# Kernel tuning notes

Measured on AMD Instinct MI355X. Metric: run time of the kernel, lower is better.

Reference implementation:

```python
import jax, jax.numpy as jnp
import numpy as np

TEMPERATURE = 0.2
HYPER_GAMMA = 0.5
EPS = 1e-12  # torch F.normalize / cosine_similarity eps guard (1e-12 / 1e-8)

def setup_inputs() -> dict:
    key = jax.random.key(0)
    k1, k2 = jax.random.split(key)
    B, D = 4096, 1024
    return {
        "emb_i": jax.random.normal(k1, (B, D), dtype=jnp.float32),
        "emb_j": jax.random.normal(k2, (B, D), dtype=jnp.float32),
    }

def _l2_normalize(x, eps=EPS):
    n = jnp.sqrt(jnp.sum(x * x, axis=1, keepdims=True))
    return x / jnp.maximum(n, eps)

def reference(emb_i, emb_j):
    B = emb_i.shape[0]
    z_i = _l2_normalize(emb_i)
    z_j = _l2_normalize(emb_j)
    # cosine similarity of unit vectors == dot product; sim[a, b] = <z_j[a], z_i[b]>
    sim = jnp.einsum('ad,bd->ab', z_j, z_i)  # [B, B]
    sim_positive = jnp.diagonal(sim)
    positives_exp = jnp.exp(-sim_positive + TEMPERATURE)
    neg_mask = 1.0 - jnp.eye(B, dtype=sim.dtype)
    negatives_exp = neg_mask * jnp.exp(sim - TEMPERATURE)
    positives_sum = jnp.sum(jnp.log1p(positives_exp)) / B
    negatives_sum = jnp.sum(jnp.log1p(negatives_exp)) / (B * (B - 1))
    return HYPER_GAMMA * positives_sum + (1.0 - HYPER_GAMMA) * negatives_sum
```

## Files before the change

kernel.cpp:

```cpp
#include <hip/hip_runtime.h>
#include <math.h>

#define B_ROWS 4096
#define D_DIM  1024
static constexpr float TEMP = 0.2f;
static constexpr float FP8_SCALE = 16.0f;
static constexpr float INV_S2 = 1.0f / 256.0f;

typedef __attribute__((ext_vector_type(4))) float f32x4;

__device__ inline unsigned char f2fp8(float f) {
    unsigned int u = __float_as_uint(f);
    unsigned int s = (u >> 24) & 0x80u;
    float af = fabsf(f);
    unsigned char b;
    if (af >= 0x1.0p-6f) {
        unsigned int au = u & 0x7fffffffu;
        unsigned int lsb = (au >> 20) & 1u;
        au += 0x7ffffu + lsb;
        int e = (int)(au >> 23) - 127 + 7;
        unsigned int m = (au >> 20) & 7u;
        if (e > 15 || (e == 15 && m > 6)) b = 0x7e;
        else b = (unsigned char)((e << 3) | m);
    } else {
        int q = (int)rintf(af * 512.0f);
        b = (unsigned char)(q >= 8 ? 0x08 : q);
    }
    return (unsigned char)(b | s);
}

__device__ inline unsigned int f2fp8x4(float4 v) {
    return (unsigned int)f2fp8(v.x)
         | ((unsigned int)f2fp8(v.y) << 8)
         | ((unsigned int)f2fp8(v.z) << 16)
         | ((unsigned int)f2fp8(v.w) << 24);
}

__device__ inline void gload_lds16(const unsigned char* g, unsigned char* l) {
    __builtin_amdgcn_global_load_lds(
        (const __attribute__((address_space(1))) unsigned int*)g,
        (__attribute__((address_space(3))) unsigned int*)l,
        16, 0, 0);
}


__global__ __launch_bounds__(256) void norm_cast_kernel(
        const float* __restrict__ emb_i, const float* __restrict__ emb_j,
        unsigned char* __restrict__ Zi8, unsigned char* __restrict__ Zj8,
        float* __restrict__ w) {
    const int tid = threadIdx.x;
    if (blockIdx.x == 0 && tid == 0) {
        w[0] = 0.0f; w[1] = 0.0f;
        ((unsigned int*)w)[2] = 0u;
    }
    const int wave = tid >> 6, lane = tid & 63;
    const int row = blockIdx.x * 4 + wave;
    const float* src; unsigned char* dst; int r;
    if (row < B_ROWS) { src = emb_i; dst = Zi8; r = row; }
    else              { src = emb_j; dst = Zj8; r = row - B_ROWS; }

    const float4* p = (const float4*)(src + (size_t)r * D_DIM);
    float4 v0 = p[lane], v1 = p[64 + lane], v2 = p[128 + lane], v3 = p[192 + lane];
    float s = v0.x*v0.x + v0.y*v0.y + v0.z*v0.z + v0.w*v0.w
            + v1.x*v1.x + v1.y*v1.y + v1.z*v1.z + v1.w*v1.w
            + v2.x*v2.x + v2.y*v2.y + v2.z*v2.z + v2.w*v2.w
            + v3.x*v3.x + v3.y*v3.y + v3.z*v3.z + v3.w*v3.w;
    #pragma unroll
    for (int m = 1; m < 64; m <<= 1) s += __shfl_xor(s, m, 64);
    const float inv = FP8_SCALE / fmaxf(sqrtf(s), 1e-12f);

    float4 a0 = {v0.x*inv, v0.y*inv, v0.z*inv, v0.w*inv};
    float4 a1 = {v1.x*inv, v1.y*inv, v1.z*inv, v1.w*inv};
    float4 a2 = {v2.x*inv, v2.y*inv, v2.z*inv, v2.w*inv};
    float4 a3 = {v3.x*inv, v3.y*inv, v3.z*inv, v3.w*inv};
    unsigned int* q = (unsigned int*)(dst + (size_t)r * D_DIM);
    q[lane]       = f2fp8x4(a0);
    q[64 + lane]  = f2fp8x4(a1);
    q[128 + lane] = f2fp8x4(a2);
    q[192 + lane] = f2fp8x4(a3);
}

__global__ __launch_bounds__(256, 2) void simloss_mfma_fp8_kernel(
        const unsigned char* __restrict__ Zi8,
        const unsigned char* __restrict__ Zj8,
        float* __restrict__ w, float* __restrict__ out) {
    __shared__ __align__(16) unsigned char lA[128 * 64];
    __shared__ __align__(16) unsigned char lB[256 * 64];
    __shared__ float rn[4], rp[4];

    const int tid  = threadIdx.x;
    const int lane = tid & 63;
    const int wave = tid >> 6;
    const int wy = wave >> 1, wx = wave & 1;
    const int rowBase = blockIdx.y * 128;
    const int colBase = blockIdx.x * 256;

    const int lrow = lane >> 2;
    const int lp   = lane & 3;
    const int lc   = (lp - (lrow >> 2)) & 3;
    const unsigned char* gA0 = Zj8 + (size_t)(rowBase + (2*wave+0)*16 + lrow) * D_DIM + lc*16;
    const unsigned char* gA1 = Zj8 + (size_t)(rowBase + (2*wave+1)*16 + lrow) * D_DIM + lc*16;
    const unsigned char* gB0 = Zi8 + (size_t)(colBase + (4*wave+0)*16 + lrow) * D_DIM + lc*16;
    const unsigned char* gB1 = Zi8 + (size_t)(colBase + (4*wave+1)*16 + lrow) * D_DIM + lc*16;
    const unsigned char* gB2 = Zi8 + (size_t)(colBase + (4*wave+2)*16 + lrow) * D_DIM + lc*16;
    const unsigned char* gB3 = Zi8 + (size_t)(colBase + (4*wave+3)*16 + lrow) * D_DIM + lc*16;
    unsigned char* sA0 = lA + (2*wave+0) * 1024;
    unsigned char* sA1 = lA + (2*wave+1) * 1024;
    unsigned char* sB0 = lB + (4*wave+0) * 1024;
    unsigned char* sB1 = lB + (4*wave+1) * 1024;
    unsigned char* sB2 = lB + (4*wave+2) * 1024;
    unsigned char* sB3 = lB + (4*wave+3) * 1024;

    const int fr = lane & 15;
    const int q4 = lane >> 4;
    const int qh = q4 >> 1, qb = q4 & 1;
    const int P0 = (qh + 0 + (fr >> 2)) & 3;
    const int P1 = (qh + 2 + (fr >> 2)) & 3;
    const unsigned char* fA0 = lA + (wy * 64 + fr) * 64 + P0 * 16 + qb * 8;
    const unsigned char* fA1 = lA + (wy * 64 + fr) * 64 + P1 * 16 + qb * 8;
    const unsigned char* fB0 = lB + (wx * 128 + fr) * 64 + P0 * 16 + qb * 8;
    const unsigned char* fB1 = lB + (wx * 128 + fr) * 64 + P1 * 16 + qb * 8;

    f32x4 acc[4][8];
    #pragma unroll
    for (int i = 0; i < 4; ++i)
        #pragma unroll
        for (int j = 0; j < 8; ++j)
            acc[i][j] = (f32x4){0.f, 0.f, 0.f, 0.f};

    for (int k0 = 0; k0 < D_DIM; k0 += 64) {
        __syncthreads();
        gload_lds16(gA0, sA0); gload_lds16(gA1, sA1);
        gload_lds16(gB0, sB0); gload_lds16(gB1, sB1);
        gload_lds16(gB2, sB2); gload_lds16(gB3, sB3);
        gA0 += 64; gA1 += 64; gB0 += 64; gB1 += 64; gB2 += 64; gB3 += 64;
        __syncthreads();

        {
            long a[4], b[8];
            #pragma unroll
            for (int i = 0; i < 4; ++i) a[i] = *(const long*)(fA0 + i * 1024);
            #pragma unroll
            for (int j = 0; j < 8; ++j) b[j] = *(const long*)(fB0 + j * 1024);
            #pragma unroll
            for (int i = 0; i < 4; ++i)
                #pragma unroll
                for (int j = 0; j < 8; ++j)
                    acc[i][j] = __builtin_amdgcn_mfma_f32_16x16x32_fp8_fp8(
                        a[i], b[j], acc[i][j], 0, 0, 0);
        }
        {
            long a[4], b[8];
            #pragma unroll
            for (int i = 0; i < 4; ++i) a[i] = *(const long*)(fA1 + i * 1024);
            #pragma unroll
            for (int j = 0; j < 8; ++j) b[j] = *(const long*)(fB1 + j * 1024);
            #pragma unroll
            for (int i = 0; i < 4; ++i)
                #pragma unroll
                for (int j = 0; j < 8; ++j)
                    acc[i][j] = __builtin_amdgcn_mfma_f32_16x16x32_fp8_fp8(
                        a[i], b[j], acc[i][j], 0, 0, 0);
        }
    }

    const int cr = q4 * 4;
    const int cc = lane & 15;
    float neg = 0.f, pos = 0.f;
    #pragma unroll
    for (int i = 0; i < 4; ++i) {
        const int abase = rowBase + wy * 64 + i * 16 + cr;
        #pragma unroll
        for (int j = 0; j < 8; ++j) {
            const int b = colBase + wx * 128 + j * 16 + cc;
            #pragma unroll
            for (int r = 0; r < 4; ++r) {
                const float x = acc[i][j][r] * INV_S2 - TEMP;
                if (abase + r == b) pos += __logf(1.0f + __expf(-x));
                else                neg += __logf(1.0f + __expf(x));
            }
        }
    }
    #pragma unroll
    for (int off = 32; off > 0; off >>= 1) {
        neg += __shfl_down(neg, off, 64);
        pos += __shfl_down(pos, off, 64);
    }
    if (lane == 0) { rn[wave] = neg; rp[wave] = pos; }
    __syncthreads();
    if (tid == 0) {
        atomicAdd(&w[1], rn[0] + rn[1] + rn[2] + rn[3]);
        if ((int)blockIdx.x == (int)(blockIdx.y >> 1))
            atomicAdd(&w[0], rp[0] + rp[1] + rp[2] + rp[3]);
        __threadfence();
        unsigned int done = atomicAdd(((unsigned int*)w) + 2, 1u);
        if (done == gridDim.x * gridDim.y - 1) {
            const float psum = atomicAdd(&w[0], 0.0f);
            const float nsum = atomicAdd(&w[1], 0.0f);
            out[0] = 0.5f * (psum / (float)B_ROWS)
                   + 0.5f * (nsum / ((float)B_ROWS * (float)(B_ROWS - 1)));
        }
    }
}

extern "C" void kernel_launch(void* const* d_in, const int* in_sizes, int n_in,
                              void* d_out, int out_size, void* d_ws, size_t ws_size,
                              hipStream_t stream) {
    const float* emb_i = (const float*)d_in[0];
    const float* emb_j = (const float*)d_in[1];
    float* w = (float*)d_ws;
    unsigned char* Zi8 = (unsigned char*)(w + 16);
    unsigned char* Zj8 = Zi8 + (size_t)B_ROWS * D_DIM;
    float* out = (float*)d_out;

    norm_cast_kernel<<<2 * B_ROWS / 4, 256, 0, stream>>>(emb_i, emb_j, Zi8, Zj8, w);
    dim3 grid(B_ROWS / 256, B_ROWS / 128);
    simloss_mfma_fp8_kernel<<<grid, 256, 0, stream>>>(Zi8, Zj8, w, out);
}
```

Measured before the change: 117.9 us.

## Switch to 32x32x64 scaled MFMA with 128-wide K tiles

Replaces the 16x16x32 fp8 MFMA with the gfx950 scaled 32x32x64 f8f6f4 MFMA, using unit scales (0x7f), and doubles the K tile staged in LDS to 128 bytes per row with a new XOR-style swizzle. The larger instruction and tile are meant to raise MFMA throughput per LDS read and halve the number of K-loop barrier iterations. In exchange LDS use doubles to 48KB per block, which may limit occupancy. The epilogue index mapping and swizzle offsets must match the 32x32 layout exactly, which is a correctness risk.

```diff
diff --git a/kernel.cpp b/kernel.cpp
--- a/kernel.cpp
+++ b/kernel.cpp
@@ -7,7 +7,8 @@
 static constexpr float FP8_SCALE = 16.0f;
 static constexpr float INV_S2 = 1.0f / 256.0f;
 
-typedef __attribute__((ext_vector_type(4))) float f32x4;
+typedef __attribute__((ext_vector_type(8))) int    i32x8;
+typedef __attribute__((ext_vector_type(16))) float f32x16;
 
 __device__ inline unsigned char f2fp8(float f) {
     unsigned int u = __float_as_uint(f);
@@ -43,6 +44,13 @@
         16, 0, 0);
 }
 
+__device__ inline i32x8 ld_frag(const unsigned char* row, int o0, int o1) {
+    union { i32x8 v; int4 q[2]; } u;
+    u.q[0] = *(const int4*)(row + o0);
+    u.q[1] = *(const int4*)(row + o1);
+    return u.v;
+}
+
 
 __global__ __launch_bounds__(256) void norm_cast_kernel(
         const float* __restrict__ emb_i, const float* __restrict__ emb_j,
@@ -80,12 +88,12 @@
     q[192 + lane] = f2fp8x4(a3);
 }
 
-__global__ __launch_bounds__(256, 2) void simloss_mfma_fp8_kernel(
+__global__ __launch_bounds__(256, 2) void simloss_mxfp8_kernel(
         const unsigned char* __restrict__ Zi8,
         const unsigned char* __restrict__ Zj8,
         float* __restrict__ w, float* __restrict__ out) {
-    __shared__ __align__(16) unsigned char lA[128 * 64];
-    __shared__ __align__(16) unsigned char lB[256 * 64];
+    __shared__ __align__(16) unsigned char lA[128 * 128];
+    __shared__ __align__(16) unsigned char lB[256 * 128];
     __shared__ float rn[4], rp[4];
 
     const int tid  = threadIdx.x;
@@ -95,96 +103,97 @@
     const int rowBase = blockIdx.y * 128;
     const int colBase = blockIdx.x * 256;
 
-    const int lrow = lane >> 2;
-    const int lp   = lane & 3;
-    const int lc   = (lp - (lrow >> 2)) & 3;
-    const unsigned char* gA0 = Zj8 + (size_t)(rowBase + (2*wave+0)*16 + lrow) * D_DIM + lc*16;
-    const unsigned char* gA1 = Zj8 + (size_t)(rowBase + (2*wave+1)*16 + lrow) * D_DIM + lc*16;
-    const unsigned char* gB0 = Zi8 + (size_t)(colBase + (4*wave+0)*16 + lrow) * D_DIM + lc*16;
-    const unsigned char* gB1 = Zi8 + (size_t)(colBase + (4*wave+1)*16 + lrow) * D_DIM + lc*16;
-    const unsigned char* gB2 = Zi8 + (size_t)(colBase + (4*wave+2)*16 + lrow) * D_DIM + lc*16;
-    const unsigned char* gB3 = Zi8 + (size_t)(colBase + (4*wave+3)*16 + lrow) * D_DIM + lc*16;
-    unsigned char* sA0 = lA + (2*wave+0) * 1024;
-    unsigned char* sA1 = lA + (2*wave+1) * 1024;
-    unsigned char* sB0 = lB + (4*wave+0) * 1024;
-    unsigned char* sB1 = lB + (4*wave+1) * 1024;
-    unsigned char* sB2 = lB + (4*wave+2) * 1024;
-    unsigned char* sB3 = lB + (4*wave+3) * 1024;
-
-    const int fr = lane & 15;
-    const int q4 = lane >> 4;
-    const int qh = q4 >> 1, qb = q4 & 1;
-    const int P0 = (qh + 0 + (fr >> 2)) & 3;
-    const int P1 = (qh + 2 + (fr >> 2)) & 3;
-    const unsigned char* fA0 = lA + (wy * 64 + fr) * 64 + P0 * 16 + qb * 8;
-    const unsigned char* fA1 = lA + (wy * 64 + fr) * 64 + P1 * 16 + qb * 8;
-    const unsigned char* fB0 = lB + (wx * 128 + fr) * 64 + P0 * 16 + qb * 8;
-    const unsigned char* fB1 = lB + (wx * 128 + fr) * 64 + P1 * 16 + qb * 8;
-
-    f32x4 acc[4][8];
-    #pragma unroll
-    for (int i = 0; i < 4; ++i)
-        #pragma unroll
-        for (int j = 0; j < 8; ++j)
-            acc[i][j] = (f32x4){0.f, 0.f, 0.f, 0.f};
-
-    for (int k0 = 0; k0 < D_DIM; k0 += 64) {
+    const int lrow = lane >> 3;
+    const int lp   = lane & 7;
+    const int lc   = (lp - lrow) & 7;
+    const unsigned char* gA[4]; unsigned char* sA[4];
+    const unsigned char* gB[8]; unsigned char* sB[8];
+    #pragma unroll
+    for (int c = 0; c < 4; ++c) {
+        gA[c] = Zj8 + (size_t)(rowBase + (4*wave + c)*8 + lrow) * D_DIM + lc*16;
+        sA[c] = lA + (4*wave + c) * 1024;
+    }
+    #pragma unroll
+    for (int c = 0; c < 8; ++c) {
+        gB[c] = Zi8 + (size_t)(colBase + (8*wave + c)*8 + lrow) * D_DIM + lc*16;
+        sB[c] = lB + (8*wave + c) * 1024;
+    }
+
+    const int r31 = lane & 31;
+    const int h   = lane >> 5;
+    int off[2][2];
+    #pragma unroll
+    for (int kb = 0; kb < 2; ++kb) {
+        off[kb][0] = ((((kb << 2) + (h << 1) + 0) + (lane & 7)) & 7) * 16;
+        off[kb][1] = ((((kb << 2) + (h << 1) + 1) + (lane & 7)) & 7) * 16;
+    }
+    const unsigned char* fA[2];
+    #pragma unroll
+    for (int ti = 0; ti < 2; ++ti) fA[ti] = lA + (wy*64 + ti*32 + r31) * 128;
+    const unsigned char* fB[4];
+    #pragma unroll
+    for (int tj = 0; tj < 4; ++tj) fB[tj] = lB + (wx*128 + tj*32 + r31) * 128;
+
+    f32x16 acc[2][4];
+    #pragma unroll
+    for (int ti = 0; ti < 2; ++ti)
+        #pragma unroll
+        for (int tj = 0; tj < 4; ++tj)
+            #pragma unroll
+            for (int r = 0; r < 16; ++r) acc[ti][tj][r] = 0.0f;
+
+    for (int k0 = 0; k0 < D_DIM; k0 += 128) {
         __syncthreads();
-        gload_lds16(gA0, sA0); gload_lds16(gA1, sA1);
-        gload_lds16(gB0, sB0); gload_lds16(gB1, sB1);
-        gload_lds16(gB2, sB2); gload_lds16(gB3, sB3);
-        gA0 += 64; gA1 += 64; gB0 += 64; gB1 += 64; gB2 += 64; gB3 += 64;
+        #pragma unroll
+        for (int c = 0; c < 4; ++c) gload_lds16(gA[c] + k0, sA[c]);
+        #pragma unroll
+        for (int c = 0; c < 8; ++c) gload_lds16(gB[c] + k0, sB[c]);
         __syncthreads();
 
-        {
-            long a[4], b[8];
-            #pragma unroll
-            for (int i = 0; i < 4; ++i) a[i] = *(const long*)(fA0 + i * 1024);
-            #pragma unroll
-            for (int j = 0; j < 8; ++j) b[j] = *(const long*)(fB0 + j * 1024);
-            #pragma unroll
-            for (int i = 0; i < 4; ++i)
+        i32x8 a[2][2];
+        #pragma unroll
+        for (int ti = 0; ti < 2; ++ti)
+            #pragma unroll
+            for (int kb = 0; kb < 2; ++kb)
+                a[ti][kb] = ld_frag(fA[ti], off[kb][0], off[kb][1]);
+
+        #pragma unroll
+        for (int tj = 0; tj < 4; ++tj) {
+            #pragma unroll
+            for (int kb = 0; kb < 2; ++kb) {
+                i32x8 b = ld_frag(fB[tj], off[kb][0], off[kb][1]);
                 #pragma unroll
-                for (int j = 0; j < 8; ++j)
-                    acc[i][j] = __builtin_amdgcn_mfma_f32_16x16x32_fp8_fp8(
-                        a[i], b[j], acc[i][j], 0, 0, 0);
-        }
-        {
-            long a[4], b[8];
-            #pragma unroll
-            for (int i = 0; i < 4; ++i) a[i] = *(const long*)(fA1 + i * 1024);
-            #pragma unroll
-            for (int j = 0; j < 8; ++j) b[j] = *(const long*)(fB1 + j * 1024);
-            #pragma unroll
-            for (int i = 0; i < 4; ++i)
-                #pragma unroll
-                for (int j = 0; j < 8; ++j)
-                    acc[i][j] = __builtin_amdgcn_mfma_f32_16x16x32_fp8_fp8(
-                        a[i], b[j], acc[i][j], 0, 0, 0);
-        }
-    }
-
-    const int cr = q4 * 4;
-    const int cc = lane & 15;
-    float neg = 0.f, pos = 0.f;
-    #pragma unroll
-    for (int i = 0; i < 4; ++i) {
-        const int abase = rowBase + wy * 64 + i * 16 + cr;
-        #pragma unroll
-        for (int j = 0; j < 8; ++j) {
-            const int b = colBase + wx * 128 + j * 16 + cc;
-            #pragma unroll
-            for (int r = 0; r < 4; ++r) {
-                const float x = acc[i][j][r] * INV_S2 - TEMP;
-                if (abase + r == b) pos += __logf(1.0f + __expf(-x));
-                else                neg += __logf(1.0f + __expf(x));
+                for (int ti = 0; ti < 2; ++ti)
+                    acc[ti][tj] = __builtin_amdgcn_mfma_scale_f32_32x32x64_f8f6f4(
+                        a[ti][kb], b, acc[ti][tj],
+                        0, 0,
+                        0, 0x7f7f7f7f,
+                        0, 0x7f7f7f7f);
             }
         }
     }
-    #pragma unroll
-    for (int off = 32; off > 0; off >>= 1) {
-        neg += __shfl_down(neg, off, 64);
-        pos += __shfl_down(pos, off, 64);
+
+    const int erow = rowBase + wy*64 + h*4;
+    const int ecol = colBase + wx*128 + r31;
+    float neg = 0.f, pos = 0.f;
+    #pragma unroll
+    for (int ti = 0; ti < 2; ++ti) {
+        #pragma unroll
+        for (int tj = 0; tj < 4; ++tj) {
+            #pragma unroll
+            for (int r = 0; r < 16; ++r) {
+                const int row = erow + ti*32 + (r & 3) + 8*(r >> 2);
+                const int col = ecol + tj*32;
+                const float x = acc[ti][tj][r] * INV_S2 - TEMP;
+                if (row == col) pos += __logf(1.0f + __expf(-x));
+                else            neg += __logf(1.0f + __expf(x));
+            }
+        }
+    }
+    #pragma unroll
+    for (int o = 32; o > 0; o >>= 1) {
+        neg += __shfl_down(neg, o, 64);
+        pos += __shfl_down(pos, o, 64);
     }
     if (lane == 0) { rn[wave] = neg; rp[wave] = pos; }
     __syncthreads();
@@ -215,5 +224,5 @@
 
     norm_cast_kernel<<<2 * B_ROWS / 4, 256, 0, stream>>>(emb_i, emb_j, Zi8, Zj8, w);
     dim3 grid(B_ROWS / 256, B_ROWS / 128);
-    simloss_mfma_fp8_kernel<<<grid, 256, 0, stream>>>(Zi8, Zj8, w, out);
-}
+    simloss_mxfp8_kernel<<<grid, 256, 0, stream>>>(Zi8, Zj8, w, out);
+}
```

Measured after the change: 278.8 us. 136% more time.
